# Kernel optimization log

Measured on AMD Instinct MI355X. Metric: run time of the kernel, lower is better.

The kernel has to match this reference:

```python
import jax, jax.numpy as jnp
import numpy as np

HEADS = 8
EPS = 1e-5


def setup_inputs() -> dict:
    key = jax.random.key(0)
    ks = jax.random.split(key, 5)
    B, C, H, W = 8, 384, 128, 128
    x = jax.random.normal(ks[0], (B, C, H, W), jnp.float32)
    ln_w = jnp.ones((C,), jnp.float32)                                # LayerNorm weight (bias=False)
    w_pconv = jax.random.normal(ks[1], (3 * C, C), jnp.float32) * 0.02   # 1x1 conv: (O, I)
    w_dconv = jax.random.normal(ks[2], (3 * C, 1, 3, 3), jnp.float32) * 0.02  # depthwise 3x3 (OIHW, groups=3C)
    w_out = jax.random.normal(ks[3], (C, C), jnp.float32) * 0.02      # output 1x1 conv: (O, I)
    alpha = jax.random.normal(ks[4], (1,), jnp.float32) * 0.1 + 1.0   # learned temperature (kept away from 0)
    return dict(x=x, ln_w=ln_w, w_pconv=w_pconv, w_dconv=w_dconv, w_out=w_out, alpha=alpha)


def reference(x, ln_w, w_pconv, w_dconv, w_out, alpha):
    B, C, H, W = x.shape
    h, d = HEADS, C // HEADS
    # LayerNorm over channel dim (bias-free)
    xt = x.transpose(0, 2, 3, 1)                      # B H W C
    mu = xt.mean(-1, keepdims=True)
    var = xt.var(-1, keepdims=True)
    xn = (xt - mu) / jnp.sqrt(var + EPS) * ln_w
    xn = xn.transpose(0, 3, 1, 2)                     # B C H W
    # 1x1 pointwise conv -> 3C channels
    qkv = jnp.einsum('bchw,oc->bohw', xn, w_pconv)
    # depthwise 3x3 conv, zero padding
    qkv = jax.lax.conv_general_dilated(
        qkv, w_dconv, window_strides=(1, 1), padding=[(1, 1), (1, 1)],
        dimension_numbers=('NCHW', 'OIHW', 'NCHW'), feature_group_count=3 * C)
    qkv = qkv.transpose(0, 2, 3, 1)                   # B H W 3C
    q, k, v = jnp.split(qkv, 3, axis=-1)              # each B H W C
    to_heads = lambda t: t.reshape(B, H * W, h, d).transpose(0, 2, 1, 3)  # B h N d
    q, k, v = map(to_heads, (q, k, v))
    # transposed (channel) attention: d x d score matrix per head
    score = jax.nn.softmax(jnp.einsum('bhni,bhnj->bhij', q, k) / alpha[0], axis=-1)
    attn = jnp.einsum('bhni,bhij->bhnj', v, score)    # B h N d
    attn = attn.transpose(0, 1, 3, 2).reshape(B, C, H, W)  # B (h d) H W
    out = jnp.einsum('bchw,oc->bohw', attn, w_out) + x
    return out
```

## Files before the change

kernel.cpp:

```cpp
#include <hip/hip_runtime.h>

typedef unsigned short u16;
typedef unsigned int u32;
typedef __bf16 bf16;
typedef bf16 bf16x8 __attribute__((ext_vector_type(8)));
typedef float f32x4 __attribute__((ext_vector_type(4)));

#define CIN 384
#define C3 1152
#define NPIX 16384
#define NB 8
#define DH 48
#define IMG 128
#define BK 32

__device__ __forceinline__ u16 f2bf(float f) {
  u32 u = __float_as_uint(f);
  u32 r = (u + 0x7fffu + ((u >> 16) & 1u)) >> 16;
  return (u16)r;
}
__device__ __forceinline__ float bf2f(u16 a) { return __uint_as_float(((u32)a) << 16); }
__device__ __forceinline__ u32 pk(u16 a, u16 b) { return (u32)a | ((u32)b << 16); }

__device__ __forceinline__ void gload16(const u16* g, u16* l) {
  __builtin_amdgcn_global_load_lds((const __attribute__((address_space(1))) void*)g,
                                   (__attribute__((address_space(3))) void*)l, 16, 0, 0);
}

__global__ __launch_bounds__(256) void k_wcvt(const float* __restrict__ wp,
                                              const float* __restrict__ wo,
                                              u16* __restrict__ wpb,
                                              u16* __restrict__ wob) {
  int i = blockIdx.x * 256 + threadIdx.x;
  if (i < C3 * CIN) wpb[i] = f2bf(wp[i]);
  if (i < CIN * CIN) wob[i] = f2bf(wo[i]);
}

__global__ __launch_bounds__(256) void k_norm(const float* __restrict__ x,
                                              const float* __restrict__ lnw,
                                              u16* __restrict__ xnt) {
  int idx = blockIdx.x * 256 + threadIdx.x;
  int b = idx >> 14, p = idx & (NPIX - 1);
  const float* xp = x + (size_t)b * CIN * NPIX + p;
  float s = 0.f, s2 = 0.f;
#pragma unroll 4
  for (int c = 0; c < CIN; ++c) {
    float v = xp[(size_t)c * NPIX];
    s += v; s2 += v * v;
  }
  float m = s * (1.f / CIN);
  float rs = rsqrtf(s2 * (1.f / CIN) - m * m + 1e-5f);
  u16* op = xnt + (size_t)idx * CIN;
  for (int c0 = 0; c0 < CIN; c0 += 16) {
    u16 t[16];
#pragma unroll
    for (int i = 0; i < 16; ++i)
      t[i] = f2bf((xp[(size_t)(c0 + i) * NPIX] - m) * rs * lnw[c0 + i]);
    uint4 v0 = make_uint4(pk(t[0], t[1]), pk(t[2], t[3]), pk(t[4], t[5]), pk(t[6], t[7]));
    uint4 v1 = make_uint4(pk(t[8], t[9]), pk(t[10], t[11]), pk(t[12], t[13]), pk(t[14], t[15]));
    *(uint4*)&op[c0] = v0;
    *(uint4*)&op[c0 + 8] = v1;
  }
}

__global__ __launch_bounds__(256) void k_pconv(const u16* __restrict__ wpb,
                                               const u16* __restrict__ xnt,
                                               u16* __restrict__ qkv_pre) {
  __shared__ u16 As[128 * BK];
  __shared__ u16 Bs[128 * BK];
  int blk = blockIdx.x;
  int pt = blk & 127;
  int ot = (blk >> 7) % 9;
  int b = blk / (9 * 128);
  int o0 = ot * 128, p0 = pt * 128;
  int tid = threadIdx.x;
  int lane = tid & 63, wave = tid >> 6;
  int ml = lane & 15, quad = lane >> 4;
  int wm = (wave & 1) * 64, wn = (wave >> 1) * 64;

  int lr = lane >> 2;
  int ck = ((lane & 3) - ((lane >> 3) & 3)) & 3;
  const u16* srcA0 = wpb + (size_t)(o0 + 32 * wave + lr) * CIN + ck * 8;
  const u16* srcA1 = srcA0 + (size_t)16 * CIN;
  const u16* srcB0 = xnt + ((size_t)((b << 14) + p0 + 32 * wave + lr)) * CIN + ck * 8;
  const u16* srcB1 = srcB0 + (size_t)16 * CIN;
  u16* dA0 = &As[(32 * wave) * BK];
  u16* dA1 = &As[(32 * wave + 16) * BK];
  u16* dB0 = &Bs[(32 * wave) * BK];
  u16* dB1 = &Bs[(32 * wave + 16) * BK];

  f32x4 acc[4][4];
#pragma unroll
  for (int i = 0; i < 4; ++i)
#pragma unroll
    for (int j = 0; j < 4; ++j) acc[i][j] = (f32x4){0.f, 0.f, 0.f, 0.f};

  for (int kc = 0; kc < CIN; kc += BK) {
    gload16(srcA0 + kc, dA0);
    gload16(srcA1 + kc, dA1);
    gload16(srcB0 + kc, dB0);
    gload16(srcB1 + kc, dB1);
    __syncthreads();
    bf16x8 af[4], bfr[4];
#pragma unroll
    for (int mt = 0; mt < 4; ++mt) {
      int rw = wm + mt * 16 + ml;
      af[mt] = *(const bf16x8*)&As[rw * BK + (((quad + (rw >> 1)) & 3) * 8)];
    }
#pragma unroll
    for (int nt = 0; nt < 4; ++nt) {
      int rw = wn + nt * 16 + ml;
      bfr[nt] = *(const bf16x8*)&Bs[rw * BK + (((quad + (rw >> 1)) & 3) * 8)];
    }
#pragma unroll
    for (int mt = 0; mt < 4; ++mt)
#pragma unroll
      for (int nt = 0; nt < 4; ++nt)
        acc[mt][nt] = __builtin_amdgcn_mfma_f32_16x16x32_bf16(af[mt], bfr[nt], acc[mt][nt], 0, 0, 0);
    __syncthreads();
  }
#pragma unroll
  for (int mt = 0; mt < 4; ++mt)
#pragma unroll
    for (int nt = 0; nt < 4; ++nt) {
      int o = o0 + wm + mt * 16 + quad * 4;
      int p = p0 + wn + nt * 16 + ml;
      size_t base = ((size_t)(b * C3 + o)) * NPIX + p;
#pragma unroll
      for (int r = 0; r < 4; ++r)
        qkv_pre[base + (size_t)r * NPIX] = f2bf(acc[mt][nt][r]);
    }
}

__global__ __launch_bounds__(256) void k_dconv(const u16* __restrict__ pre,
                                               const float* __restrict__ wd,
                                               u16* __restrict__ post) {
  int bidx = blockIdx.x;
  int cg = bidx >> 1;
  int half = bidx & 1;
  int ch = cg % C3;
  int tid = threadIdx.x;
  int y0 = half * 64 + (tid >> 4) * 4;
  int x0 = (tid & 15) * 8;
  const u16* pb = pre + (size_t)cg * NPIX;
  const float* wc = wd + ch * 9;
  float w[9];
#pragma unroll
  for (int i = 0; i < 9; ++i) w[i] = wc[i];

  uint4 v[6];
  u16 eL[6], eR[6];
#pragma unroll
  for (int r = 0; r < 6; ++r) {
    int yy = y0 + r - 1;
    bool ok = ((unsigned)yy < (unsigned)IMG);
    const u16* row = pb + yy * IMG + x0;
    v[r] = ok ? *(const uint4*)row : make_uint4(0u, 0u, 0u, 0u);
    eL[r] = (ok && x0 > 0) ? row[-1] : (u16)0;
    eR[r] = (ok && x0 < IMG - 8) ? row[8] : (u16)0;
  }

  float acc[4][8];
#pragma unroll
  for (int j = 0; j < 4; ++j)
#pragma unroll
    for (int i = 0; i < 8; ++i) acc[j][i] = 0.f;

#pragma unroll
  for (int r = 0; r < 6; ++r) {
    float rr[10];
    const u16* pv = (const u16*)&v[r];
    rr[0] = bf2f(eL[r]);
    rr[9] = bf2f(eR[r]);
#pragma unroll
    for (int i = 0; i < 8; ++i) rr[i + 1] = bf2f(pv[i]);
#pragma unroll
    for (int j = 0; j < 4; ++j) {
      int ky = r - j;
      if (ky < 0 || ky > 2) continue;
      float w0 = w[ky * 3 + 0], w1 = w[ky * 3 + 1], w2 = w[ky * 3 + 2];
#pragma unroll
      for (int i = 0; i < 8; ++i)
        acc[j][i] += rr[i] * w0 + rr[i + 1] * w1 + rr[i + 2] * w2;
    }
  }
#pragma unroll
  for (int j = 0; j < 4; ++j) {
    u16 o[8];
#pragma unroll
    for (int i = 0; i < 8; ++i) o[i] = f2bf(acc[j][i]);
    uint4 ov = make_uint4(pk(o[0], o[1]), pk(o[2], o[3]), pk(o[4], o[5]), pk(o[6], o[7]));
    *(uint4*)(post + (size_t)cg * NPIX + (y0 + j) * IMG + x0) = ov;
  }
}

__global__ __launch_bounds__(64) void k_score(const u16* __restrict__ post,
                                              float* __restrict__ partial) {
  int blk = blockIdx.x;
  int chunk = blk & 63, bh = blk >> 6;
  int b = bh >> 3, h = bh & 7;
  int lane = threadIdx.x;
  int ml = lane & 15, quad = lane >> 4;
  int n0 = chunk * 256;
  const u16* qp[3];
  const u16* kp[3];
#pragma unroll
  for (int t = 0; t < 3; ++t) {
    qp[t] = post + ((size_t)(b * C3 + h * DH + t * 16 + ml)) * NPIX + n0 + quad * 8;
    kp[t] = post + ((size_t)(b * C3 + CIN + h * DH + t * 16 + ml)) * NPIX + n0 + quad * 8;
  }
  f32x4 acc[3][3];
#pragma unroll
  for (int i = 0; i < 3; ++i)
#pragma unroll
    for (int j = 0; j < 3; ++j) acc[i][j] = (f32x4){0.f, 0.f, 0.f, 0.f};
  for (int ks = 0; ks < 256; ks += 32) {
    bf16x8 qf[3], kf[3];
#pragma unroll
    for (int t = 0; t < 3; ++t) {
      qf[t] = *(const bf16x8*)(qp[t] + ks);
      kf[t] = *(const bf16x8*)(kp[t] + ks);
    }
#pragma unroll
    for (int it = 0; it < 3; ++it)
#pragma unroll
      for (int jt = 0; jt < 3; ++jt)
        acc[it][jt] = __builtin_amdgcn_mfma_f32_16x16x32_bf16(qf[it], kf[jt], acc[it][jt], 0, 0, 0);
  }
  float* pp = partial + (size_t)blk * (DH * DH);
#pragma unroll
  for (int it = 0; it < 3; ++it)
#pragma unroll
    for (int jt = 0; jt < 3; ++jt)
#pragma unroll
      for (int r = 0; r < 4; ++r)
        pp[(it * 16 + quad * 4 + r) * DH + jt * 16 + ml] = acc[it][jt][r];
}

__global__ __launch_bounds__(256) void k_softmax(const float* __restrict__ partial,
                                                 const float* __restrict__ alpha,
                                                 u16* __restrict__ scoreT) {
  __shared__ float sc[DH * DH];
  __shared__ float pr[DH * DH];
  int bh = blockIdx.x, tid = threadIdx.x;
  const float* pp = partial + (size_t)bh * 64 * (DH * DH);
  for (int e = tid; e < DH * DH; e += 256) {
    float s = 0.f;
    for (int c = 0; c < 64; ++c) s += pp[(size_t)c * (DH * DH) + e];
    sc[e] = s;
  }
  __syncthreads();
  float inv_a = 1.0f / alpha[0];
  if (tid < DH) {
    int i = tid;
    float mx = -1e30f;
    for (int j = 0; j < DH; ++j) mx = fmaxf(mx, sc[i * DH + j] * inv_a);
    float sum = 0.f;
    for (int j = 0; j < DH; ++j) {
      float e = __expf(sc[i * DH + j] * inv_a - mx);
      pr[i * DH + j] = e;
      sum += e;
    }
    float r = 1.f / sum;
    for (int j = 0; j < DH; ++j) pr[i * DH + j] *= r;
  }
  __syncthreads();
  u16* st = scoreT + (size_t)bh * DH * 64;
  for (int e = tid; e < DH * 64; e += 256) {
    int j = e >> 6, i = e & 63;
    st[e] = f2bf(i < DH ? pr[i * DH + j] : 0.f);
  }
}

#define VS_LD 72
__global__ __launch_bounds__(256) void k_attnv(const u16* __restrict__ post,
                                               const u16* __restrict__ scoreT,
                                               u16* __restrict__ attn_t) {
  __shared__ u16 Vs[128 * VS_LD];
  int blk = blockIdx.x;
  int pt = blk & 127, h = (blk >> 7) & 7, b = blk >> 10;
  int p0 = pt * 128;
  int tid = threadIdx.x, lane = tid & 63, wave = tid >> 6;
  int ml = lane & 15, quad = lane >> 4;
  {
    int n = tid & 127;
    int i0 = (tid >> 7) * 32;
    size_t vbase = ((size_t)(b * C3 + 2 * CIN + h * DH)) * NPIX + p0 + n;
    u16 t[32];
#pragma unroll
    for (int i = 0; i < 32; ++i) {
      int ic = i0 + i;
      int icc = ic < DH ? ic : (DH - 1);
      t[i] = post[vbase + (size_t)icc * NPIX];
    }
#pragma unroll
    for (int q2 = 0; q2 < 4; ++q2) {
      uint4 v = make_uint4(pk(t[q2 * 8 + 0], t[q2 * 8 + 1]), pk(t[q2 * 8 + 2], t[q2 * 8 + 3]),
                           pk(t[q2 * 8 + 4], t[q2 * 8 + 5]), pk(t[q2 * 8 + 6], t[q2 * 8 + 7]));
      *(uint4*)&Vs[n * VS_LD + i0 + q2 * 8] = v;
    }
  }
  __syncthreads();
  const u16* sT = scoreT + (size_t)(b * 8 + h) * (DH * 64);
  int wn = wave * 32;
  f32x4 acc[3][2];
#pragma unroll
  for (int i = 0; i < 3; ++i)
#pragma unroll
    for (int j = 0; j < 2; ++j) acc[i][j] = (f32x4){0.f, 0.f, 0.f, 0.f};
#pragma unroll
  for (int ks = 0; ks < 2; ++ks) {
    bf16x8 a3[3], b2[2];
#pragma unroll
    for (int mt = 0; mt < 3; ++mt)
      a3[mt] = *(const bf16x8*)&sT[(mt * 16 + ml) * 64 + ks * 32 + quad * 8];
#pragma unroll
    for (int nt = 0; nt < 2; ++nt)
      b2[nt] = *(const bf16x8*)&Vs[(wn + nt * 16 + ml) * VS_LD + ks * 32 + quad * 8];
#pragma unroll
    for (int mt = 0; mt < 3; ++mt)
#pragma unroll
      for (int nt = 0; nt < 2; ++nt)
        acc[mt][nt] = __builtin_amdgcn_mfma_f32_16x16x32_bf16(a3[mt], b2[nt], acc[mt][nt], 0, 0, 0);
  }
#pragma unroll
  for (int mt = 0; mt < 3; ++mt)
#pragma unroll
    for (int nt = 0; nt < 2; ++nt) {
      int j0 = mt * 16 + quad * 4;
      int n = wn + nt * 16 + ml;
      u16 o4[4];
#pragma unroll
      for (int r = 0; r < 4; ++r) o4[r] = f2bf(acc[mt][nt][r]);
      uint2 ov = make_uint2(pk(o4[0], o4[1]), pk(o4[2], o4[3]));
      *(uint2*)&attn_t[((size_t)((b << 14) + p0 + n)) * CIN + h * DH + j0] = ov;
    }
}

__global__ __launch_bounds__(256) void k_out(const u16* __restrict__ wob,
                                             const u16* __restrict__ attn_t,
                                             const float* __restrict__ x,
                                             float* __restrict__ out) {
  __shared__ u16 As[128 * BK];
  __shared__ u16 Bs[128 * BK];
  int blk = blockIdx.x;
  int pt = blk & 127;
  int ot = (blk >> 7) % 3;
  int b = blk / (3 * 128);
  int o0 = ot * 128, p0 = pt * 128;
  int tid = threadIdx.x;
  int lane = tid & 63, wave = tid >> 6;
  int ml = lane & 15, quad = lane >> 4;
  int wm = (wave & 1) * 64, wn = (wave >> 1) * 64;

  int lr = lane >> 2;
  int ck = ((lane & 3) - ((lane >> 3) & 3)) & 3;
  const u16* srcA0 = wob + (size_t)(o0 + 32 * wave + lr) * CIN + ck * 8;
  const u16* srcA1 = srcA0 + (size_t)16 * CIN;
  const u16* srcB0 = attn_t + ((size_t)((b << 14) + p0 + 32 * wave + lr)) * CIN + ck * 8;
  const u16* srcB1 = srcB0 + (size_t)16 * CIN;
  u16* dA0 = &As[(32 * wave) * BK];
  u16* dA1 = &As[(32 * wave + 16) * BK];
  u16* dB0 = &Bs[(32 * wave) * BK];
  u16* dB1 = &Bs[(32 * wave + 16) * BK];

  f32x4 acc[4][4];
#pragma unroll
  for (int i = 0; i < 4; ++i)
#pragma unroll
    for (int j = 0; j < 4; ++j) acc[i][j] = (f32x4){0.f, 0.f, 0.f, 0.f};

  for (int kc = 0; kc < CIN; kc += BK) {
    gload16(srcA0 + kc, dA0);
    gload16(srcA1 + kc, dA1);
    gload16(srcB0 + kc, dB0);
    gload16(srcB1 + kc, dB1);
    __syncthreads();
    bf16x8 af[4], bfr[4];
#pragma unroll
    for (int mt = 0; mt < 4; ++mt) {
      int rw = wm + mt * 16 + ml;
      af[mt] = *(const bf16x8*)&As[rw * BK + (((quad + (rw >> 1)) & 3) * 8)];
    }
#pragma unroll
    for (int nt = 0; nt < 4; ++nt) {
      int rw = wn + nt * 16 + ml;
      bfr[nt] = *(const bf16x8*)&Bs[rw * BK + (((quad + (rw >> 1)) & 3) * 8)];
    }
#pragma unroll
    for (int mt = 0; mt < 4; ++mt)
#pragma unroll
      for (int nt = 0; nt < 4; ++nt)
        acc[mt][nt] = __builtin_amdgcn_mfma_f32_16x16x32_bf16(af[mt], bfr[nt], acc[mt][nt], 0, 0, 0);
    __syncthreads();
  }
#pragma unroll
  for (int mt = 0; mt < 4; ++mt)
#pragma unroll
    for (int nt = 0; nt < 4; ++nt) {
      int o = o0 + wm + mt * 16 + quad * 4;
      int p = p0 + wn + nt * 16 + ml;
      size_t base = ((size_t)(b * CIN + o)) * NPIX + p;
#pragma unroll
      for (int r = 0; r < 4; ++r) {
        size_t gi = base + (size_t)r * NPIX;
        out[gi] = acc[mt][nt][r] + x[gi];
      }
    }
}

extern "C" void kernel_launch(void* const* d_in, const int* in_sizes, int n_in,
                              void* d_out, int out_size, void* d_ws, size_t ws_size,
                              hipStream_t stream) {
  const float* x = (const float*)d_in[0];
  const float* lnw = (const float*)d_in[1];
  const float* wp = (const float*)d_in[2];
  const float* wd = (const float*)d_in[3];
  const float* wo = (const float*)d_in[4];
  const float* alpha = (const float*)d_in[5];
  float* out = (float*)d_out;

  char* ws = (char*)d_ws;
  u16* wpb = (u16*)ws;
  u16* wob = (u16*)(ws + 884736);
  u16* qkv_pre = (u16*)(ws + 1179648);
  u16* attn_t = qkv_pre;
  float* partial = (float*)(ws + 1179648 + 100663296);
  u16* scoreT = (u16*)(ws + 1179648 + 100663296 + 37748736);
  u16* qkv_post = (u16*)(ws + 303169536);
  u16* xnt = (u16*)d_out;

  hipLaunchKernelGGL(k_wcvt, dim3(1728), dim3(256), 0, stream, wp, wo, wpb, wob);
  hipLaunchKernelGGL(k_norm, dim3(512), dim3(256), 0, stream, x, lnw, xnt);
  hipLaunchKernelGGL(k_pconv, dim3(NB * 9 * 128), dim3(256), 0, stream, wpb, xnt, qkv_pre);
  hipLaunchKernelGGL(k_dconv, dim3(NB * C3 * 2), dim3(256), 0, stream, qkv_pre, wd, qkv_post);
  hipLaunchKernelGGL(k_score, dim3(64 * 64), dim3(64), 0, stream, qkv_post, partial);
  hipLaunchKernelGGL(k_softmax, dim3(64), dim3(256), 0, stream, partial, alpha, scoreT);
  hipLaunchKernelGGL(k_attnv, dim3(NB * 8 * 128), dim3(256), 0, stream, qkv_post, scoreT, attn_t);
  hipLaunchKernelGGL(k_out, dim3(NB * 3 * 128), dim3(256), 0, stream, wob, attn_t, x, out);
}
```

Baseline: 1.006 ms.

## Double-buffer LDS staging in pointwise GEMMs and shuffle dconv halos

The two 1x1-conv GEMM kernels now use two LDS buffers, so the global-to-LDS load for the next K chunk is issued before the MFMA work on the current chunk, with one barrier per iteration instead of two. This is meant to hide global load latency behind the matrix math. Separately, the depthwise conv gets its left and right halo elements from neighbouring lanes via wave shuffles instead of extra scalar global loads. The cost is twice the LDS per block, which may lower occupancy.

```diff
diff --git a/kernel.cpp b/kernel.cpp
--- a/kernel.cpp
+++ b/kernel.cpp
@@ -13,6 +13,7 @@
 #define DH 48
 #define IMG 128
 #define BK 32
+#define NKS (CIN / BK)
 
 __device__ __forceinline__ u16 f2bf(float f) {
   u32 u = __float_as_uint(f);
@@ -66,8 +67,8 @@
 __global__ __launch_bounds__(256) void k_pconv(const u16* __restrict__ wpb,
                                                const u16* __restrict__ xnt,
                                                u16* __restrict__ qkv_pre) {
-  __shared__ u16 As[128 * BK];
-  __shared__ u16 Bs[128 * BK];
+  __shared__ u16 As[2][128 * BK];
+  __shared__ u16 Bs[2][128 * BK];
   int blk = blockIdx.x;
   int pt = blk & 127;
   int ot = (blk >> 7) % 9;
@@ -84,10 +85,7 @@
   const u16* srcA1 = srcA0 + (size_t)16 * CIN;
   const u16* srcB0 = xnt + ((size_t)((b << 14) + p0 + 32 * wave + lr)) * CIN + ck * 8;
   const u16* srcB1 = srcB0 + (size_t)16 * CIN;
-  u16* dA0 = &As[(32 * wave) * BK];
-  u16* dA1 = &As[(32 * wave + 16) * BK];
-  u16* dB0 = &Bs[(32 * wave) * BK];
-  u16* dB1 = &Bs[(32 * wave + 16) * BK];
+  int dOff0 = (32 * wave) * BK, dOff1 = (32 * wave + 16) * BK;
 
   f32x4 acc[4][4];
 #pragma unroll
@@ -95,30 +93,40 @@
 #pragma unroll
     for (int j = 0; j < 4; ++j) acc[i][j] = (f32x4){0.f, 0.f, 0.f, 0.f};
 
-  for (int kc = 0; kc < CIN; kc += BK) {
-    gload16(srcA0 + kc, dA0);
-    gload16(srcA1 + kc, dA1);
-    gload16(srcB0 + kc, dB0);
-    gload16(srcB1 + kc, dB1);
-    __syncthreads();
+  auto stg = [&](int bi, int kc) {
+    gload16(srcA0 + kc, &As[bi][dOff0]);
+    gload16(srcA1 + kc, &As[bi][dOff1]);
+    gload16(srcB0 + kc, &Bs[bi][dOff0]);
+    gload16(srcB1 + kc, &Bs[bi][dOff1]);
+  };
+  auto cmp = [&](int bi) {
     bf16x8 af[4], bfr[4];
 #pragma unroll
     for (int mt = 0; mt < 4; ++mt) {
       int rw = wm + mt * 16 + ml;
-      af[mt] = *(const bf16x8*)&As[rw * BK + (((quad + (rw >> 1)) & 3) * 8)];
+      af[mt] = *(const bf16x8*)&As[bi][rw * BK + (((quad + (rw >> 1)) & 3) * 8)];
     }
 #pragma unroll
     for (int nt = 0; nt < 4; ++nt) {
       int rw = wn + nt * 16 + ml;
-      bfr[nt] = *(const bf16x8*)&Bs[rw * BK + (((quad + (rw >> 1)) & 3) * 8)];
+      bfr[nt] = *(const bf16x8*)&Bs[bi][rw * BK + (((quad + (rw >> 1)) & 3) * 8)];
     }
 #pragma unroll
     for (int mt = 0; mt < 4; ++mt)
 #pragma unroll
       for (int nt = 0; nt < 4; ++nt)
         acc[mt][nt] = __builtin_amdgcn_mfma_f32_16x16x32_bf16(af[mt], bfr[nt], acc[mt][nt], 0, 0, 0);
+  };
+
+  stg(0, 0);
+  __syncthreads();
+  for (int t = 0; t < NKS - 1; ++t) {
+    stg((t & 1) ^ 1, (t + 1) * BK);
+    cmp(t & 1);
     __syncthreads();
   }
+  cmp((NKS - 1) & 1);
+
 #pragma unroll
   for (int mt = 0; mt < 4; ++mt)
 #pragma unroll
@@ -140,8 +148,9 @@
   int half = bidx & 1;
   int ch = cg % C3;
   int tid = threadIdx.x;
+  int xl = tid & 15;
   int y0 = half * 64 + (tid >> 4) * 4;
-  int x0 = (tid & 15) * 8;
+  int x0 = xl * 8;
   const u16* pb = pre + (size_t)cg * NPIX;
   const float* wc = wd + ch * 9;
   float w[9];
@@ -149,15 +158,12 @@
   for (int i = 0; i < 9; ++i) w[i] = wc[i];
 
   uint4 v[6];
-  u16 eL[6], eR[6];
 #pragma unroll
   for (int r = 0; r < 6; ++r) {
     int yy = y0 + r - 1;
     bool ok = ((unsigned)yy < (unsigned)IMG);
     const u16* row = pb + yy * IMG + x0;
     v[r] = ok ? *(const uint4*)row : make_uint4(0u, 0u, 0u, 0u);
-    eL[r] = (ok && x0 > 0) ? row[-1] : (u16)0;
-    eR[r] = (ok && x0 < IMG - 8) ? row[8] : (u16)0;
   }
 
   float acc[4][8];
@@ -168,10 +174,12 @@
 
 #pragma unroll
   for (int r = 0; r < 6; ++r) {
+    u32 lw = (u32)__shfl_up((int)v[r].w, 1);
+    u32 rw = (u32)__shfl_down((int)v[r].x, 1);
     float rr[10];
     const u16* pv = (const u16*)&v[r];
-    rr[0] = bf2f(eL[r]);
-    rr[9] = bf2f(eR[r]);
+    rr[0] = (xl > 0) ? bf2f((u16)(lw >> 16)) : 0.f;
+    rr[9] = (xl < 15) ? bf2f((u16)(rw & 0xffffu)) : 0.f;
 #pragma unroll
     for (int i = 0; i < 8; ++i) rr[i + 1] = bf2f(pv[i]);
 #pragma unroll
@@ -341,8 +349,8 @@
                                              const u16* __restrict__ attn_t,
                                              const float* __restrict__ x,
                                              float* __restrict__ out) {
-  __shared__ u16 As[128 * BK];
-  __shared__ u16 Bs[128 * BK];
+  __shared__ u16 As[2][128 * BK];
+  __shared__ u16 Bs[2][128 * BK];
   int blk = blockIdx.x;
   int pt = blk & 127;
   int ot = (blk >> 7) % 3;
@@ -359,10 +367,7 @@
   const u16* srcA1 = srcA0 + (size_t)16 * CIN;
   const u16* srcB0 = attn_t + ((size_t)((b << 14) + p0 + 32 * wave + lr)) * CIN + ck * 8;
   const u16* srcB1 = srcB0 + (size_t)16 * CIN;
-  u16* dA0 = &As[(32 * wave) * BK];
-  u16* dA1 = &As[(32 * wave + 16) * BK];
-  u16* dB0 = &Bs[(32 * wave) * BK];
-  u16* dB1 = &Bs[(32 * wave + 16) * BK];
+  int dOff0 = (32 * wave) * BK, dOff1 = (32 * wave + 16) * BK;
 
   f32x4 acc[4][4];
 #pragma unroll
@@ -370,30 +375,40 @@
 #pragma unroll
     for (int j = 0; j < 4; ++j) acc[i][j] = (f32x4){0.f, 0.f, 0.f, 0.f};
 
-  for (int kc = 0; kc < CIN; kc += BK) {
-    gload16(srcA0 + kc, dA0);
-    gload16(srcA1 + kc, dA1);
-    gload16(srcB0 + kc, dB0);
-    gload16(srcB1 + kc, dB1);
-    __syncthreads();
+  auto stg = [&](int bi, int kc) {
+    gload16(srcA0 + kc, &As[bi][dOff0]);
+    gload16(srcA1 + kc, &As[bi][dOff1]);
+    gload16(srcB0 + kc, &Bs[bi][dOff0]);
+    gload16(srcB1 + kc, &Bs[bi][dOff1]);
+  };
+  auto cmp = [&](int bi) {
     bf16x8 af[4], bfr[4];
 #pragma unroll
     for (int mt = 0; mt < 4; ++mt) {
       int rw = wm + mt * 16 + ml;
-      af[mt] = *(const bf16x8*)&As[rw * BK + (((quad + (rw >> 1)) & 3) * 8)];
+      af[mt] = *(const bf16x8*)&As[bi][rw * BK + (((quad + (rw >> 1)) & 3) * 8)];
     }
 #pragma unroll
     for (int nt = 0; nt < 4; ++nt) {
       int rw = wn + nt * 16 + ml;
-      bfr[nt] = *(const bf16x8*)&Bs[rw * BK + (((quad + (rw >> 1)) & 3) * 8)];
+      bfr[nt] = *(const bf16x8*)&Bs[bi][rw * BK + (((quad + (rw >> 1)) & 3) * 8)];
     }
 #pragma unroll
     for (int mt = 0; mt < 4; ++mt)
 #pragma unroll
       for (int nt = 0; nt < 4; ++nt)
         acc[mt][nt] = __builtin_amdgcn_mfma_f32_16x16x32_bf16(af[mt], bfr[nt], acc[mt][nt], 0, 0, 0);
+  };
+
+  stg(0, 0);
+  __syncthreads();
+  for (int t = 0; t < NKS - 1; ++t) {
+    stg((t & 1) ^ 1, (t + 1) * BK);
+    cmp(t & 1);
     __syncthreads();
   }
+  cmp((NKS - 1) & 1);
+
 #pragma unroll
   for (int mt = 0; mt < 4; ++mt)
 #pragma unroll
```

New measurement: 1.022 ms. About the same (+1.6%).
